# Optimization experiments

Measured on AMD Instinct MI355X. Metric: run time of the kernel, lower is better.

Reference implementation:

```python
import jax, jax.numpy as jnp
import numpy as np

B, N, D = 512, 64, 2
NODE_H, EDGE_H, STEPS, JH = 32, 32, 2, 16
OMEGA = 1.0
ENV_WIDTH = 1.0


def setup_inputs() -> dict:
    key = jax.random.key(0)
    ks = jax.random.split(key, 24)

    def p(k, shape, scale=0.1):
        return jax.random.normal(k, shape, dtype=jnp.float32) * scale

    inp = {}
    inp["x"] = jax.random.normal(ks[0], (B, N, D), dtype=jnp.float32)
    inp["spin"] = jax.random.randint(ks[1], (N,), 0, 2)
    inp["node_W"] = p(ks[2], (NODE_H, D))
    inp["edge_W"] = p(ks[3], (EDGE_H, 1 + 2 * NODE_H))
    inp["rho_ve_W"] = p(ks[4], (STEPS, EDGE_H, NODE_H))
    inp["eu_W1"] = p(ks[5], (STEPS, EDGE_H, 3 * EDGE_H))
    inp["eu_b1"] = p(ks[6], (STEPS, EDGE_H))
    inp["eu_W2"] = p(ks[7], (STEPS, EDGE_H, EDGE_H))
    inp["eu_b2"] = p(ks[8], (STEPS, EDGE_H))
    inp["rho_ev_W"] = p(ks[9], (STEPS, NODE_H, EDGE_H))
    inp["nu_W1"] = p(ks[10], (STEPS, NODE_H, 2 * NODE_H))
    inp["nu_b1"] = p(ks[11], (STEPS, NODE_H))
    inp["nu_W2"] = p(ks[12], (STEPS, NODE_H, NODE_H))
    inp["nu_b2"] = p(ks[13], (STEPS, NODE_H))
    inp["dx_W"] = p(ks[14], (D, NODE_H))
    inp["bf_scale_raw"] = jnp.asarray(np.log(np.exp(1.0) - 1.0), dtype=jnp.float32)
    inp["f_W1"] = p(ks[15], (JH, NODE_H + EDGE_H + 1))
    inp["f_b1"] = p(ks[16], (JH,))
    inp["f_W2"] = p(ks[17], (1, JH))
    inp["f_b2"] = p(ks[18], (1,))
    return inp


def reference(x, spin, node_W, edge_W, rho_ve_W, eu_W1, eu_b1, eu_W2, eu_b2,
              rho_ev_W, nu_W1, nu_b1, nu_W2, nu_b2, dx_W, bf_scale_raw,
              f_W1, f_b1, f_W2, f_b2):
    ii, jj = np.triu_indices(N, k=1)  # upper-triangular pair indices (static)
    x_sc = x * (OMEGA ** 0.5)
    h_v = x_sc @ node_W.T                                   # (B,N,NODE_H)
    r_vec = x_sc[:, None, :, :] - x_sc[:, :, None, :]       # (B,N,N,D)
    r2 = jnp.sum(r_vec * r_vec, axis=-1, keepdims=True)     # (B,N,N,1)
    r1 = jnp.sqrt(r2 + 1e-12)
    h_i = jnp.broadcast_to(h_v[:, :, None, :], (B, N, N, NODE_H))
    h_j = jnp.broadcast_to(h_v[:, None, :, :], (B, N, N, NODE_H))
    h_e = jnp.concatenate([r1, h_i, h_j], axis=-1) @ edge_W.T  # (B,N,N,EDGE_H)

    for s in range(STEPS):
        v = h_v @ rho_ve_W[s].T                              # (B,N,EDGE_H)
        v_i = jnp.broadcast_to(v[:, :, None, :], h_e.shape)
        v_j = jnp.broadcast_to(v[:, None, :, :], h_e.shape)
        ein = jnp.concatenate([h_e, v_i, v_j], axis=-1)      # (B,N,N,3*EDGE_H)
        h_e = jnp.tanh(ein @ eu_W1[s].T + eu_b1[s]) @ eu_W2[s].T + eu_b2[s]
        m_v = jnp.sum(h_e @ rho_ev_W[s].T, axis=2)           # sum aggregation over j
        nin = jnp.concatenate([h_v, m_v], axis=-1)
        h_v = jnp.tanh(nin @ nu_W1[s].T + nu_b1[s]) @ nu_W2[s].T + nu_b2[s]

    scale = jax.nn.softplus(bf_scale_raw)
    dx = scale * jnp.tanh(h_v @ dx_W.T)                      # (B,N,D)

    h_v_mean = h_v.mean(axis=1)                              # (B,NODE_H)
    h_e_mean = h_e[:, ii, jj, :].mean(axis=1)                # (B,EDGE_H)
    rdist = jnp.sqrt(r2[..., 0] + 1e-12)
    mask = 1.0 - jnp.eye(N, dtype=x.dtype)
    r2_mean = jnp.sum(rdist * mask, axis=(1, 2)) / float(N * (N - 1))
    f_in = jnp.concatenate([h_v_mean, h_e_mean, r2_mean[:, None]], axis=-1)
    f_nn = jnp.tanh(f_in @ f_W1.T + f_b1) @ f_W2.T + f_b2    # (B,1)

    ell2 = ENV_WIDTH / max(OMEGA, 1e-12)
    envelope = jnp.exp(-0.5 * jnp.sum(x * x, axis=(1, 2)) / ell2)[:, None]
    diff = x[:, ii, :] - x[:, jj, :]
    r_phys = jnp.sqrt(jnp.sum(diff * diff, axis=-1) + 1e-30)  # (B,P)
    same = (spin[ii] == spin[jj]).astype(x.dtype)
    gamma_para = 1.0 / (D + 1)
    gamma_apara = 1.0 / max(D - 1, 1)
    gamma = same * gamma_para + (1.0 - same) * gamma_apara
    cusp_len = 1.0 / (OMEGA ** 0.5)
    cusp = jnp.sum(gamma * r_phys / (1.0 + r_phys / cusp_len), axis=-1, keepdims=True)
    f = f_nn * envelope + 0.2 * cusp
    return dx, f
```

## Files before the change

kernel.cpp:

```cpp
#include <hip/hip_runtime.h>
#include <math.h>


constexpr float SQRT_OMEGA  = 1.0f;
constexpr float ELL2        = 1.0f;
constexpr float GAMMA_PARA  = 1.0f/3.0f;
constexpr float GAMMA_APARA = 1.0f;
constexpr float C2LOG2E     = 2.8853900817779268f;

typedef float f32x16 __attribute__((ext_vector_type(16)));
typedef short s16x8  __attribute__((ext_vector_type(8)));
typedef unsigned u32x2 __attribute__((ext_vector_type(2)));

__device__ __forceinline__ float ftanh(float x) {
    float e = __expf(2.0f*x);
    return 1.0f - 2.0f/(e + 1.0f);
}

__device__ __forceinline__ float tanhE(float q) {
    float E, r;
    asm("v_exp_f32 %0, %1" : "=v"(E) : "v"(q));
    float d = 1.0f + E;
    asm("v_rcp_f32 %0, %1" : "=v"(r) : "v"(d));
    return fmaf(-2.0f, r, 1.0f);
}

__device__ __forceinline__ unsigned cvtpk(float lo, float hi) {
    unsigned r;
    asm("v_cvt_pk_bf16_f32 %0, %1, %2" : "=v"(r) : "v"(lo), "v"(hi));
    return r;
}

__device__ __forceinline__ s16x8 frag4(unsigned a, unsigned b, unsigned c, unsigned d) {
    union { unsigned u[4]; s16x8 v; } x;
    x.u[0]=a; x.u[1]=b; x.u[2]=c; x.u[3]=d;
    return x.v;
}

#define MFMA(a,b,c) __builtin_amdgcn_mfma_f32_32x32x16_bf16(a,b,c,0,0,0)

__global__ void k_weights(const float* __restrict__ edge_W, const float* __restrict__ rho_ve_W,
                          const float* __restrict__ eu_W1, const float* __restrict__ eu_W2,
                          const float* __restrict__ eu_b2, const float* __restrict__ rho_ev_W,
                          const float* __restrict__ nu_W1, const float* __restrict__ nu_W2,
                          float* __restrict__ MiT0, float* __restrict__ MjT0,
                          float* __restrict__ NiT1, float* __restrict__ NjT1,
                          float* __restrict__ K1T,  float* __restrict__ R0T,
                          float* __restrict__ R1T,  float* __restrict__ rb0,
                          float* __restrict__ rb1,  float* __restrict__ u0c1,
                          float* __restrict__ W1T0, float* __restrict__ W1T1,
                          float* __restrict__ W2T0, float* __restrict__ W2T1)
{
    int t = blockIdx.x*256 + threadIdx.x;
    if (t >= 1024) return;
    int k = t >> 5, eo = t & 31;
    float mi=0.f, mj=0.f, ni=0.f, nj=0.f, k1=0.f;
    for (int a = 0; a < 32; ++a) {
        float w1h = eu_W1[eo*96 + a];
        mi += w1h*edge_W[a*65 + 1 + k];
        mj += w1h*edge_W[a*65 + 33 + k];
        float r0 = rho_ve_W[a*32 + k];
        mi += eu_W1[eo*96 + 32 + a]*r0;
        mj += eu_W1[eo*96 + 64 + a]*r0;
        float r1v = rho_ve_W[1024 + a*32 + k];
        ni += eu_W1[3072 + eo*96 + 32 + a]*r1v;
        nj += eu_W1[3072 + eo*96 + 64 + a]*r1v;
        k1 += eu_W1[3072 + eo*96 + a]*eu_W2[a*32 + k];
    }
    MiT0[t]=mi; MjT0[t]=mj; NiT1[t]=ni; NjT1[t]=nj;
    K1T[t]=k1*C2LOG2E;
    {
        int a = t >> 5, kk = t & 31;
        float r0a=0.f, r1a=0.f;
        for (int e = 0; e < 32; ++e) {
            r0a += rho_ev_W[a*32 + e]*eu_W2[e*32 + kk];
            r1a += rho_ev_W[1024 + a*32 + e]*eu_W2[1024 + e*32 + kk];
        }
        R0T[kk*32 + a] = r0a;
        R1T[kk*32 + a] = r1a;
    }
    {
        int kk = t >> 5, hh = t & 31;
        W1T0[t]        = nu_W1[hh*64 + kk]*C2LOG2E;
        W1T0[1024 + t] = nu_W1[hh*64 + 32 + kk]*C2LOG2E;
        W1T1[t]        = nu_W1[2048 + hh*64 + kk]*C2LOG2E;
        W1T1[1024 + t] = nu_W1[2048 + hh*64 + 32 + kk]*C2LOG2E;
        W2T0[t]        = nu_W2[hh*32 + kk];
        W2T1[t]        = nu_W2[1024 + hh*32 + kk];
    }
    if (t < 32) {
        float u=0.f, c=0.f, b0=0.f, b1v=0.f;
        for (int kk = 0; kk < 32; ++kk) {
            u   += eu_W1[t*96 + kk]*edge_W[kk*65];
            c   += eu_W1[3072 + t*96 + kk]*eu_b2[kk];
            b0  += rho_ev_W[t*32 + kk]*eu_b2[kk];
            b1v += rho_ev_W[1024 + t*32 + kk]*eu_b2[32 + kk];
        }
        u0c1[t] = u*C2LOG2E;
        u0c1[32+t] = c;
        rb0[t] = 64.f*b0; rb1[t] = 64.f*b1v;
    }
}

__launch_bounds__(256)
__global__ void k_fused(const float* __restrict__ x, const int* __restrict__ spin,
                        const float* __restrict__ node_W,
                        const float* __restrict__ eu_b1, const float* __restrict__ eu_W2,
                        const float* __restrict__ eu_b2,
                        const float* __restrict__ MiT0, const float* __restrict__ MjT0,
                        const float* __restrict__ NiT1, const float* __restrict__ NjT1,
                        const float* __restrict__ K1T,  const float* __restrict__ u0c1,
                        const float* __restrict__ R0T,  const float* __restrict__ R1T,
                        const float* __restrict__ rb0,  const float* __restrict__ rb1,
                        const float* __restrict__ W1T0, const float* __restrict__ W1T1,
                        const float* __restrict__ W2T0, const float* __restrict__ W2T1,
                        const float* __restrict__ nu_b1, const float* __restrict__ nu_b2,
                        const float* __restrict__ dx_W, const float* __restrict__ bf_scale,
                        const float* __restrict__ f_W1, const float* __restrict__ f_b1,
                        const float* __restrict__ f_W2, const float* __restrict__ f_b2,
                        float* __restrict__ dx_out, float* __restrict__ f_out)
{
    constexpr int X    = 0;
    constexpr int TI0  = 128;
    constexpr int TJ0  = 2432;
    constexpr int HV   = 4736;
    constexpr int SS   = 6848;
    constexpr int MM   = 8960;
    constexpr int HD   = 11072;
    constexpr int TI1  = MM;
    constexpr int TJ1  = HD;
    constexpr int PART = 128;
    constexpr int RED  = 392;
    constexpr int T1F  = 648;
    constexpr int HVM  = 680;
    constexpr int HEM  = 712;
    __shared__ __align__(16) float sm[13376];
    __shared__ int sp[64];

    const int tid = threadIdx.x;
    const int b   = blockIdx.x;
    const int i   = tid & 63;
    const int c   = tid >> 6;
    const int h   = i >> 5;
    const int n   = i & 31;

    if (tid < 128) sm[X + tid] = x[b*128 + tid]*SQRT_OMEGA;
    if (tid < 64)  sp[tid] = spin[tid];
    __syncthreads();

    for (int out = tid; out < 2048; out += 256) {
        int nn = out >> 5, k = out & 31;
        sm[HV + nn*33 + k] = sm[X + 2*nn]*node_W[k*2] + sm[X + 2*nn + 1]*node_W[k*2+1];
    }
    __syncthreads();

    for (int out = tid; out < 2048; out += 256) {
        int nn = out & 63, e = out >> 6;
        float ai = eu_b1[e], aj = 0.f;
        #pragma unroll
        for (int k = 0; k < 32; ++k) {
            float hvv = sm[HV + nn*33 + k];
            ai += MiT0[k*32 + e]*hvv;
            aj += MjT0[k*32 + e]*hvv;
        }
        sm[TI0 + nn*36 + e] = ai*C2LOG2E;
        sm[TJ0 + nn*36 + e] = aj*C2LOG2E;
    }
    __syncthreads();

    const float xi0 = sm[X + 2*i], xi1 = sm[X + 2*i + 1];

    {
        float ti0v[32];
        #pragma unroll
        for (int q = 0; q < 8; ++q) {
            float4 v = *(const float4*)&sm[TI0 + i*36 + 4*q];
            ti0v[4*q]=v.x; ti0v[4*q+1]=v.y; ti0v[4*q+2]=v.z; ti0v[4*q+3]=v.w;
        }
        float S0[32];
        #pragma unroll
        for (int e = 0; e < 32; ++e) S0[e] = 0.f;
        #pragma unroll 1
        for (int jl = 0; jl < 16; ++jl) {
            const int j = c*16 + jl;
            float d0 = sm[X + 2*j] - xi0;
            float d1 = sm[X + 2*j + 1] - xi1;
            float r1 = sqrtf(d0*d0 + d1*d1 + 1e-12f);
            float tj0v[32];
            #pragma unroll
            for (int q = 0; q < 8; ++q) {
                float4 v = *(const float4*)&sm[TJ0 + j*36 + 4*q];
                tj0v[4*q]=v.x; tj0v[4*q+1]=v.y; tj0v[4*q+2]=v.z; tj0v[4*q+3]=v.w;
            }
            #pragma unroll
            for (int e = 0; e < 32; ++e)
                S0[e] += tanhE(fmaf(r1, u0c1[e], ti0v[e] + tj0v[e]));
        }
        __syncthreads();
        for (int cc = 0; cc < 4; ++cc) {
            if (c == cc) {
                #pragma unroll
                for (int e = 0; e < 32; ++e) {
                    if (cc == 0) sm[SS + i*33 + e]  = S0[e];
                    else         sm[SS + i*33 + e] += S0[e];
                }
            }
            __syncthreads();
        }
    }

    for (int out = tid; out < 2048; out += 256) {
        int nn = out >> 5, a = out & 31;
        float acc = rb0[a];
        #pragma unroll
        for (int k = 0; k < 32; ++k) acc += sm[SS + nn*33 + k]*R0T[k*32 + a];
        sm[MM + nn*33 + a] = acc;
    }
    __syncthreads();
    for (int out = tid; out < 2048; out += 256) {
        int nn = out >> 5, hh = out & 31;
        float acc = nu_b1[hh]*C2LOG2E;
        #pragma unroll
        for (int k = 0; k < 32; ++k) acc += sm[HV + nn*33 + k]*W1T0[k*32 + hh];
        #pragma unroll
        for (int k = 0; k < 32; ++k) acc += sm[MM + nn*33 + k]*W1T0[(32+k)*32 + hh];
        sm[HD + nn*33 + hh] = tanhE(acc);
    }
    __syncthreads();
    for (int out = tid; out < 2048; out += 256) {
        int nn = out >> 5, oo = out & 31;
        float acc = nu_b2[oo];
        #pragma unroll
        for (int k = 0; k < 32; ++k) acc += sm[HD + nn*33 + k]*W2T0[k*32 + oo];
        sm[HV + nn*33 + oo] = acc;
    }
    __syncthreads();

    for (int out = tid; out < 2048; out += 256) {
        int nn = out & 63, e = out >> 6;
        float ai = eu_b1[32 + e] + u0c1[32 + e], aj = 0.f;
        #pragma unroll
        for (int k = 0; k < 32; ++k) {
            float hvv = sm[HV + nn*33 + k];
            ai += NiT1[k*32 + e]*hvv;
            aj += NjT1[k*32 + e]*hvv;
        }
        sm[TI1 + e*65 + nn] = ai*C2LOG2E;
        sm[TJ1 + nn*36 + e] = aj*C2LOG2E;
    }
    __syncthreads();

    {
        s16x8 B1f, B2f;
        {
            unsigned bw[8];
            #pragma unroll
            for (int v = 0; v < 4; ++v) {
                bw[v]   = cvtpk(K1T[(8*h + 2*v)*32 + n],      K1T[(8*h + 2*v + 1)*32 + n]);
                bw[4+v] = cvtpk(K1T[(16 + 8*h + 2*v)*32 + n], K1T[(16 + 8*h + 2*v + 1)*32 + n]);
            }
            B1f = frag4(bw[0],bw[1],bw[2],bw[3]);
            B2f = frag4(bw[4],bw[5],bw[6],bw[7]);
        }
        float ti0v[32];
        #pragma unroll
        for (int q = 0; q < 8; ++q) {
            float4 v = *(const float4*)&sm[TI0 + i*36 + 4*q];
            ti0v[4*q]=v.x; ti0v[4*q+1]=v.y; ti0v[4*q+2]=v.z; ti0v[4*q+3]=v.w;
        }
        float ti1a[16], ti1b[16];
        #pragma unroll
        for (int r = 0; r < 16; ++r) {
            int m = (r&3) + 8*(r>>2) + 4*h;
            ti1a[r] = sm[TI1 + n*65 + m];
            ti1b[r] = sm[TI1 + n*65 + 32 + m];
        }

        float S1a[16], S1b[16];
        #pragma unroll
        for (int r = 0; r < 16; ++r) { S1a[r] = 0.f; S1b[r] = 0.f; }
        float t1acc0 = 0.f, t1acc1 = 0.f;

        #pragma unroll 1
        for (int jl = 0; jl < 16; ++jl) {
            const int j = c*16 + jl;
            float d0 = sm[X + 2*j] - xi0;
            float d1 = sm[X + 2*j + 1] - xi1;
            float r1 = sqrtf(d0*d0 + d1*d1 + 1e-12f);

            float tj0v[32];
            #pragma unroll
            for (int q = 0; q < 8; ++q) {
                float4 v = *(const float4*)&sm[TJ0 + j*36 + 4*q];
                tj0v[4*q]=v.x; tj0v[4*q+1]=v.y; tj0v[4*q+2]=v.z; tj0v[4*q+3]=v.w;
            }
            unsigned w[16];
            #pragma unroll
            for (int q = 0; q < 16; ++q) {
                int e0 = 2*q, e1 = 2*q + 1;
                float ta = tanhE(fmaf(r1, u0c1[e0], ti0v[e0] + tj0v[e0]));
                float tb = tanhE(fmaf(r1, u0c1[e1], ti0v[e1] + tj0v[e1]));
                w[q] = cvtpk(ta, tb);
            }
            unsigned a10[4], a11[4], a20[4], a21[4];
            #pragma unroll
            for (int v = 0; v < 4; ++v) {
                u32x2 ra = __builtin_amdgcn_permlane32_swap(w[v],   w[4+v],  false, false);
                a10[v] = ra[0]; a11[v] = ra[1];
                u32x2 rb = __builtin_amdgcn_permlane32_swap(w[8+v], w[12+v], false, false);
                a20[v] = rb[0]; a21[v] = rb[1];
            }
            float tj1v = sm[TJ1 + j*36 + n];
            f32x16 acc0, acc1;
            #pragma unroll
            for (int r = 0; r < 16; ++r) {
                acc0[r] = ti1a[r] + tj1v;
                acc1[r] = ti1b[r] + tj1v;
            }
            acc0 = MFMA(frag4(a10[0],a10[1],a10[2],a10[3]), B1f, acc0);
            acc0 = MFMA(frag4(a20[0],a20[1],a20[2],a20[3]), B2f, acc0);
            acc1 = MFMA(frag4(a11[0],a11[1],a11[2],a11[3]), B1f, acc1);
            acc1 = MFMA(frag4(a21[0],a21[1],a21[2],a21[3]), B2f, acc1);
            #pragma unroll
            for (int r = 0; r < 16; ++r) {
                int m = (r&3) + 8*(r>>2) + 4*h;
                float t1a = tanhE(acc0[r]);
                float t1b = tanhE(acc1[r]);
                S1a[r] += t1a;
                S1b[r] += t1b;
                if (j > m)      t1acc0 += t1a;
                if (j > 32 + m) t1acc1 += t1b;
            }
        }
        __syncthreads();

        {
            float tf = t1acc0 + t1acc1;
            tf += __shfl_xor(tf, 32, 64);
            if (i < 32) sm[PART + c*33 + i] = tf;
        }
        for (int cc = 0; cc < 4; ++cc) {
            if (c == cc) {
                #pragma unroll
                for (int r = 0; r < 16; ++r) {
                    int m = (r&3) + 8*(r>>2) + 4*h;
                    if (cc == 0) {
                        sm[SS + m*33 + n]        = S1a[r];
                        sm[SS + (32+m)*33 + n]   = S1b[r];
                    } else {
                        sm[SS + m*33 + n]       += S1a[r];
                        sm[SS + (32+m)*33 + n]  += S1b[r];
                    }
                }
            }
            __syncthreads();
        }
        if (tid < 32) {
            sm[T1F + tid] = sm[PART + tid] + sm[PART + 33 + tid]
                          + sm[PART + 66 + tid] + sm[PART + 99 + tid];
        }
        __syncthreads();
    }

    for (int out = tid; out < 2048; out += 256) {
        int nn = out >> 5, a = out & 31;
        float acc = rb1[a];
        #pragma unroll
        for (int k = 0; k < 32; ++k) acc += sm[SS + nn*33 + k]*R1T[k*32 + a];
        sm[MM + nn*33 + a] = acc;
    }
    __syncthreads();
    for (int out = tid; out < 2048; out += 256) {
        int nn = out >> 5, hh = out & 31;
        float acc = nu_b1[32 + hh]*C2LOG2E;
        #pragma unroll
        for (int k = 0; k < 32; ++k) acc += sm[HV + nn*33 + k]*W1T1[k*32 + hh];
        #pragma unroll
        for (int k = 0; k < 32; ++k) acc += sm[MM + nn*33 + k]*W1T1[(32+k)*32 + hh];
        sm[HD + nn*33 + hh] = tanhE(acc);
    }
    __syncthreads();
    for (int out = tid; out < 2048; out += 256) {
        int nn = out >> 5, oo = out & 31;
        float acc = nu_b2[32 + oo];
        #pragma unroll
        for (int k = 0; k < 32; ++k) acc += sm[HD + nn*33 + k]*W2T1[k*32 + oo];
        sm[MM + nn*33 + oo] = acc;
    }
    __syncthreads();

    if (tid < 128) {
        int nn = tid >> 1, d = tid & 1;
        float scale = log1pf(__expf(bf_scale[0]));
        float a = 0.f;
        #pragma unroll
        for (int k = 0; k < 32; ++k) a += sm[MM + nn*33 + k]*dx_W[d*32 + k];
        dx_out[(b*64 + nn)*2 + d] = scale*ftanh(a);
    }
    {
        int e = tid & 31, g = tid >> 5;
        float p = 0.f;
        #pragma unroll
        for (int r = 0; r < 8; ++r) p += sm[MM + (g*8 + r)*33 + e];
        sm[PART + g*33 + e] = p;
    }
    __syncthreads();
    if (tid < 32) {
        float s = 0.f;
        #pragma unroll
        for (int g = 0; g < 8; ++g) s += sm[PART + g*33 + tid];
        sm[HVM + tid] = s*(1.0f/64.0f);
        float he = 0.f;
        #pragma unroll
        for (int k = 0; k < 32; ++k) he += eu_W2[1024 + tid*32 + k]*sm[T1F + k];
        sm[HEM + tid] = he*(1.0f/2016.0f) + eu_b2[32 + tid];
    }

    float rsum = 0.f, cusp = 0.f, env = 0.f;
    for (int idx = tid; idx < 4096; idx += 256) {
        int ii = idx >> 6, jj = idx & 63;
        if (ii < jj) {
            float d0 = sm[X + ii*2] - sm[X + jj*2];
            float d1 = sm[X + ii*2 + 1] - sm[X + jj*2 + 1];
            float r2 = d0*d0 + d1*d1;
            rsum += sqrtf(r2 + 1e-12f);
            float rp = sqrtf(r2 + 1e-30f);
            float gamma = (sp[ii] == sp[jj]) ? GAMMA_PARA : GAMMA_APARA;
            cusp += gamma*rp/(1.0f + rp*SQRT_OMEGA);
        }
    }
    if (tid < 128) { float v = sm[X + tid]; env = v*v; }

    auto blockReduce = [&](float v) -> float {
        sm[RED + tid] = v; __syncthreads();
        for (int s = 128; s > 0; s >>= 1) {
            if (tid < s) sm[RED + tid] += sm[RED + tid + s];
            __syncthreads();
        }
        float r = sm[RED]; __syncthreads(); return r;
    };
    float rtot = blockReduce(rsum);
    float ctot = blockReduce(cusp);
    float etot = blockReduce(env);

    if (tid < 16) {
        float r2m = rtot*(1.0f/2016.0f);
        float envelope = __expf(-0.5f*etot/ELL2);
        float acc = f_b1[tid];
        #pragma unroll
        for (int m2 = 0; m2 < 32; ++m2) acc += sm[HVM + m2]*f_W1[tid*65 + m2];
        #pragma unroll
        for (int m2 = 0; m2 < 32; ++m2) acc += sm[HEM + m2]*f_W1[tid*65 + 32 + m2];
        acc += r2m*f_W1[tid*65 + 64];
        float v = ftanh(acc)*f_W2[tid];
        v += __shfl_xor(v, 8, 64);
        v += __shfl_xor(v, 4, 64);
        v += __shfl_xor(v, 2, 64);
        v += __shfl_xor(v, 1, 64);
        if (tid == 0) f_out[b] = (v + f_b2[0])*envelope + 0.2f*ctot;
    }
}

extern "C" void kernel_launch(void* const* d_in, const int* in_sizes, int n_in,
                              void* d_out, int out_size, void* d_ws, size_t ws_size,
                              hipStream_t stream)
{
    (void)in_sizes; (void)n_in; (void)out_size; (void)ws_size;
    const float* x         = (const float*)d_in[0];
    const int*   spin      = (const int*)d_in[1];
    const float* node_W    = (const float*)d_in[2];
    const float* edge_W    = (const float*)d_in[3];
    const float* rho_ve_W  = (const float*)d_in[4];
    const float* eu_W1     = (const float*)d_in[5];
    const float* eu_b1     = (const float*)d_in[6];
    const float* eu_W2     = (const float*)d_in[7];
    const float* eu_b2     = (const float*)d_in[8];
    const float* rho_ev_W  = (const float*)d_in[9];
    const float* nu_W1     = (const float*)d_in[10];
    const float* nu_b1     = (const float*)d_in[11];
    const float* nu_W2     = (const float*)d_in[12];
    const float* nu_b2     = (const float*)d_in[13];
    const float* dx_W      = (const float*)d_in[14];
    const float* bf_scale  = (const float*)d_in[15];
    const float* f_W1      = (const float*)d_in[16];
    const float* f_b1      = (const float*)d_in[17];
    const float* f_W2      = (const float*)d_in[18];
    const float* f_b2      = (const float*)d_in[19];

    float* ws    = (float*)d_ws;
    float* MiT0  = ws;
    float* MjT0  = MiT0 + 1024;
    float* NiT1  = MjT0 + 1024;
    float* NjT1  = NiT1 + 1024;
    float* K1T   = NjT1 + 1024;
    float* R0T   = K1T  + 1024;
    float* R1T   = R0T  + 1024;
    float* W1T0  = R1T  + 1024;
    float* W1T1  = W1T0 + 2048;
    float* W2T0  = W1T1 + 2048;
    float* W2T1  = W2T0 + 1024;
    float* rb0   = W2T1 + 1024;
    float* rb1   = rb0  + 32;
    float* u0c1  = rb1  + 32;

    float* dxout = (float*)d_out;
    float* fout  = dxout + 512*64*2;

    k_weights<<<4, 256, 0, stream>>>(edge_W, rho_ve_W, eu_W1, eu_W2, eu_b2, rho_ev_W,
                                     nu_W1, nu_W2,
                                     MiT0, MjT0, NiT1, NjT1, K1T, R0T, R1T,
                                     rb0, rb1, u0c1, W1T0, W1T1, W2T0, W2T1);
    k_fused<<<512, 256, 0, stream>>>(x, spin, node_W, eu_b1, eu_W2, eu_b2,
                                     MiT0, MjT0, NiT1, NjT1, K1T, u0c1,
                                     R0T, R1T, rb0, rb1, W1T0, W1T1, W2T0, W2T1,
                                     nu_b1, nu_b2, dx_W, bf_scale,
                                     f_W1, f_b1, f_W2, f_b2, dxout, fout);
}
```

Before: 208.8 us.

## Fold weight-precompute kernel into fused kernel, computing combined weights per block in LDS

Removes the separate k_weights launch and its workspace. Each of the 512 blocks now recomputes the combined edge-update weight matrices (Mi/Mj, Ni/Nj, K1, u0/c1) into shared memory and applies rho_ev, eu_W2 and nu weights directly instead of using pre-fused products. This drops one kernel launch and the dependency between the two kernels, but every block now does redundant weight matmuls that read global memory, and it adds extra matmul passes and barriers.

```diff
diff --git a/kernel.cpp b/kernel.cpp
--- a/kernel.cpp
+++ b/kernel.cpp
@@ -39,83 +39,22 @@
 
 #define MFMA(a,b,c) __builtin_amdgcn_mfma_f32_32x32x16_bf16(a,b,c,0,0,0)
 
-__global__ void k_weights(const float* __restrict__ edge_W, const float* __restrict__ rho_ve_W,
-                          const float* __restrict__ eu_W1, const float* __restrict__ eu_W2,
-                          const float* __restrict__ eu_b2, const float* __restrict__ rho_ev_W,
-                          const float* __restrict__ nu_W1, const float* __restrict__ nu_W2,
-                          float* __restrict__ MiT0, float* __restrict__ MjT0,
-                          float* __restrict__ NiT1, float* __restrict__ NjT1,
-                          float* __restrict__ K1T,  float* __restrict__ R0T,
-                          float* __restrict__ R1T,  float* __restrict__ rb0,
-                          float* __restrict__ rb1,  float* __restrict__ u0c1,
-                          float* __restrict__ W1T0, float* __restrict__ W1T1,
-                          float* __restrict__ W2T0, float* __restrict__ W2T1)
-{
-    int t = blockIdx.x*256 + threadIdx.x;
-    if (t >= 1024) return;
-    int k = t >> 5, eo = t & 31;
-    float mi=0.f, mj=0.f, ni=0.f, nj=0.f, k1=0.f;
-    for (int a = 0; a < 32; ++a) {
-        float w1h = eu_W1[eo*96 + a];
-        mi += w1h*edge_W[a*65 + 1 + k];
-        mj += w1h*edge_W[a*65 + 33 + k];
-        float r0 = rho_ve_W[a*32 + k];
-        mi += eu_W1[eo*96 + 32 + a]*r0;
-        mj += eu_W1[eo*96 + 64 + a]*r0;
-        float r1v = rho_ve_W[1024 + a*32 + k];
-        ni += eu_W1[3072 + eo*96 + 32 + a]*r1v;
-        nj += eu_W1[3072 + eo*96 + 64 + a]*r1v;
-        k1 += eu_W1[3072 + eo*96 + a]*eu_W2[a*32 + k];
-    }
-    MiT0[t]=mi; MjT0[t]=mj; NiT1[t]=ni; NjT1[t]=nj;
-    K1T[t]=k1*C2LOG2E;
-    {
-        int a = t >> 5, kk = t & 31;
-        float r0a=0.f, r1a=0.f;
-        for (int e = 0; e < 32; ++e) {
-            r0a += rho_ev_W[a*32 + e]*eu_W2[e*32 + kk];
-            r1a += rho_ev_W[1024 + a*32 + e]*eu_W2[1024 + e*32 + kk];
-        }
-        R0T[kk*32 + a] = r0a;
-        R1T[kk*32 + a] = r1a;
-    }
-    {
-        int kk = t >> 5, hh = t & 31;
-        W1T0[t]        = nu_W1[hh*64 + kk]*C2LOG2E;
-        W1T0[1024 + t] = nu_W1[hh*64 + 32 + kk]*C2LOG2E;
-        W1T1[t]        = nu_W1[2048 + hh*64 + kk]*C2LOG2E;
-        W1T1[1024 + t] = nu_W1[2048 + hh*64 + 32 + kk]*C2LOG2E;
-        W2T0[t]        = nu_W2[hh*32 + kk];
-        W2T1[t]        = nu_W2[1024 + hh*32 + kk];
-    }
-    if (t < 32) {
-        float u=0.f, c=0.f, b0=0.f, b1v=0.f;
-        for (int kk = 0; kk < 32; ++kk) {
-            u   += eu_W1[t*96 + kk]*edge_W[kk*65];
-            c   += eu_W1[3072 + t*96 + kk]*eu_b2[kk];
-            b0  += rho_ev_W[t*32 + kk]*eu_b2[kk];
-            b1v += rho_ev_W[1024 + t*32 + kk]*eu_b2[32 + kk];
-        }
-        u0c1[t] = u*C2LOG2E;
-        u0c1[32+t] = c;
-        rb0[t] = 64.f*b0; rb1[t] = 64.f*b1v;
-    }
-}
-
 __launch_bounds__(256)
 __global__ void k_fused(const float* __restrict__ x, const int* __restrict__ spin,
                         const float* __restrict__ node_W,
-                        const float* __restrict__ eu_b1, const float* __restrict__ eu_W2,
+                        const float* __restrict__ edge_W,
+                        const float* __restrict__ rho_ve_W,
+                        const float* __restrict__ eu_W1,
+                        const float* __restrict__ eu_b1,
+                        const float* __restrict__ eu_W2,
                         const float* __restrict__ eu_b2,
-                        const float* __restrict__ MiT0, const float* __restrict__ MjT0,
-                        const float* __restrict__ NiT1, const float* __restrict__ NjT1,
-                        const float* __restrict__ K1T,  const float* __restrict__ u0c1,
-                        const float* __restrict__ R0T,  const float* __restrict__ R1T,
-                        const float* __restrict__ rb0,  const float* __restrict__ rb1,
-                        const float* __restrict__ W1T0, const float* __restrict__ W1T1,
-                        const float* __restrict__ W2T0, const float* __restrict__ W2T1,
-                        const float* __restrict__ nu_b1, const float* __restrict__ nu_b2,
-                        const float* __restrict__ dx_W, const float* __restrict__ bf_scale,
+                        const float* __restrict__ rho_ev_W,
+                        const float* __restrict__ nu_W1,
+                        const float* __restrict__ nu_b1,
+                        const float* __restrict__ nu_W2,
+                        const float* __restrict__ nu_b2,
+                        const float* __restrict__ dx_W,
+                        const float* __restrict__ bf_scale,
                         const float* __restrict__ f_W1, const float* __restrict__ f_b1,
                         const float* __restrict__ f_W2, const float* __restrict__ f_b2,
                         float* __restrict__ dx_out, float* __restrict__ f_out)
@@ -129,12 +68,13 @@
     constexpr int HD   = 11072;
     constexpr int TI1  = MM;
     constexpr int TJ1  = HD;
+    constexpr int U0C1 = 13376;
     constexpr int PART = 128;
     constexpr int RED  = 392;
     constexpr int T1F  = 648;
     constexpr int HVM  = 680;
     constexpr int HEM  = 712;
-    __shared__ __align__(16) float sm[13376];
+    __shared__ __align__(16) float sm[13440];
     __shared__ int sp[64];
 
     const int tid = threadIdx.x;
@@ -152,6 +92,31 @@
         int nn = out >> 5, k = out & 31;
         sm[HV + nn*33 + k] = sm[X + 2*nn]*node_W[k*2] + sm[X + 2*nn + 1]*node_W[k*2+1];
     }
+
+    for (int out = tid; out < 2048; out += 256) {
+        int tb = out >> 10, idx = out & 1023;
+        int eo = idx >> 5, k = idx & 31;
+        float acc = 0.f;
+        if (tb == 0) {
+            for (int a = 0; a < 32; ++a)
+                acc += eu_W1[eo*96 + a]*edge_W[a*65 + 1 + k]
+                     + eu_W1[eo*96 + 32 + a]*rho_ve_W[a*32 + k];
+        } else {
+            for (int a = 0; a < 32; ++a)
+                acc += eu_W1[eo*96 + a]*edge_W[a*65 + 33 + k]
+                     + eu_W1[eo*96 + 64 + a]*rho_ve_W[a*32 + k];
+        }
+        sm[MM + tb*1024 + eo*32 + k] = acc;
+    }
+    if (tid < 32) {
+        float u = 0.f, cc1 = 0.f;
+        for (int kk = 0; kk < 32; ++kk) {
+            u   += eu_W1[tid*96 + kk]*edge_W[kk*65];
+            cc1 += eu_W1[3072 + tid*96 + kk]*eu_b2[kk];
+        }
+        sm[U0C1 + tid]      = u*C2LOG2E;
+        sm[U0C1 + 32 + tid] = cc1;
+    }
     __syncthreads();
 
     for (int out = tid; out < 2048; out += 256) {
@@ -160,8 +125,8 @@
         #pragma unroll
         for (int k = 0; k < 32; ++k) {
             float hvv = sm[HV + nn*33 + k];
-            ai += MiT0[k*32 + e]*hvv;
-            aj += MjT0[k*32 + e]*hvv;
+            ai += sm[MM + e*32 + k]*hvv;
+            aj += sm[MM + 1024 + e*32 + k]*hvv;
         }
         sm[TI0 + nn*36 + e] = ai*C2LOG2E;
         sm[TJ0 + nn*36 + e] = aj*C2LOG2E;
@@ -194,7 +159,7 @@
             }
             #pragma unroll
             for (int e = 0; e < 32; ++e)
-                S0[e] += tanhE(fmaf(r1, u0c1[e], ti0v[e] + tj0v[e]));
+                S0[e] += tanhE(fmaf(r1, sm[U0C1 + e], ti0v[e] + tj0v[e]));
         }
         __syncthreads();
         for (int cc = 0; cc < 4; ++cc) {
@@ -210,43 +175,75 @@
     }
 
     for (int out = tid; out < 2048; out += 256) {
+        int nn = out >> 5, e = out & 31;
+        float acc = 64.f*eu_b2[e];
+        #pragma unroll
+        for (int k = 0; k < 32; ++k) acc += sm[SS + nn*33 + k]*eu_W2[e*32 + k];
+        sm[MM + nn*33 + e] = acc;
+    }
+    __syncthreads();
+    for (int out = tid; out < 2048; out += 256) {
         int nn = out >> 5, a = out & 31;
-        float acc = rb0[a];
-        #pragma unroll
-        for (int k = 0; k < 32; ++k) acc += sm[SS + nn*33 + k]*R0T[k*32 + a];
-        sm[MM + nn*33 + a] = acc;
+        float acc = 0.f;
+        #pragma unroll
+        for (int e = 0; e < 32; ++e) acc += rho_ev_W[a*32 + e]*sm[MM + nn*33 + e];
+        sm[HD + nn*33 + a] = acc;
     }
     __syncthreads();
     for (int out = tid; out < 2048; out += 256) {
         int nn = out >> 5, hh = out & 31;
-        float acc = nu_b1[hh]*C2LOG2E;
-        #pragma unroll
-        for (int k = 0; k < 32; ++k) acc += sm[HV + nn*33 + k]*W1T0[k*32 + hh];
-        #pragma unroll
-        for (int k = 0; k < 32; ++k) acc += sm[MM + nn*33 + k]*W1T0[(32+k)*32 + hh];
-        sm[HD + nn*33 + hh] = tanhE(acc);
+        float acc = nu_b1[hh];
+        #pragma unroll
+        for (int k = 0; k < 32; ++k) acc += sm[HV + nn*33 + k]*nu_W1[hh*64 + k];
+        #pragma unroll
+        for (int k = 0; k < 32; ++k) acc += sm[HD + nn*33 + k]*nu_W1[hh*64 + 32 + k];
+        sm[SS + nn*33 + hh] = tanhE(acc*C2LOG2E);
     }
     __syncthreads();
     for (int out = tid; out < 2048; out += 256) {
         int nn = out >> 5, oo = out & 31;
         float acc = nu_b2[oo];
         #pragma unroll
-        for (int k = 0; k < 32; ++k) acc += sm[HD + nn*33 + k]*W2T0[k*32 + oo];
+        for (int k = 0; k < 32; ++k) acc += sm[SS + nn*33 + k]*nu_W2[oo*32 + k];
         sm[HV + nn*33 + oo] = acc;
     }
     __syncthreads();
 
     for (int out = tid; out < 2048; out += 256) {
+        int tb = out >> 10, idx = out & 1023;
+        int eo = idx >> 5, k = idx & 31;
+        float acc = 0.f;
+        if (tb == 0) {
+            for (int a = 0; a < 32; ++a)
+                acc += eu_W1[3072 + eo*96 + 32 + a]*rho_ve_W[1024 + a*32 + k];
+        } else {
+            for (int a = 0; a < 32; ++a)
+                acc += eu_W1[3072 + eo*96 + 64 + a]*rho_ve_W[1024 + a*32 + k];
+        }
+        sm[SS + tb*1024 + eo*32 + k] = acc;
+    }
+    __syncthreads();
+
+    for (int out = tid; out < 2048; out += 256) {
         int nn = out & 63, e = out >> 6;
-        float ai = eu_b1[32 + e] + u0c1[32 + e], aj = 0.f;
+        float ai = eu_b1[32 + e] + sm[U0C1 + 32 + e], aj = 0.f;
         #pragma unroll
         for (int k = 0; k < 32; ++k) {
             float hvv = sm[HV + nn*33 + k];
-            ai += NiT1[k*32 + e]*hvv;
-            aj += NjT1[k*32 + e]*hvv;
+            ai += sm[SS + e*32 + k]*hvv;
+            aj += sm[SS + 1024 + e*32 + k]*hvv;
         }
         sm[TI1 + e*65 + nn] = ai*C2LOG2E;
         sm[TJ1 + nn*36 + e] = aj*C2LOG2E;
+    }
+    __syncthreads();
+
+    for (int out = tid; out < 1024; out += 256) {
+        int eo = out & 31, k = out >> 5;
+        float acc = 0.f;
+        for (int a = 0; a < 32; ++a)
+            acc += eu_W1[3072 + eo*96 + a]*eu_W2[a*32 + k];
+        sm[SS + k*32 + eo] = acc*C2LOG2E;
     }
     __syncthreads();
 
@@ -256,8 +253,8 @@
             unsigned bw[8];
             #pragma unroll
             for (int v = 0; v < 4; ++v) {
-                bw[v]   = cvtpk(K1T[(8*h + 2*v)*32 + n],      K1T[(8*h + 2*v + 1)*32 + n]);
-                bw[4+v] = cvtpk(K1T[(16 + 8*h + 2*v)*32 + n], K1T[(16 + 8*h + 2*v + 1)*32 + n]);
+                bw[v]   = cvtpk(sm[SS + (8*h + 2*v)*32 + n],      sm[SS + (8*h + 2*v + 1)*32 + n]);
+                bw[4+v] = cvtpk(sm[SS + (16 + 8*h + 2*v)*32 + n], sm[SS + (16 + 8*h + 2*v + 1)*32 + n]);
             }
             B1f = frag4(bw[0],bw[1],bw[2],bw[3]);
             B2f = frag4(bw[4],bw[5],bw[6],bw[7]);
@@ -298,8 +295,8 @@
             #pragma unroll
             for (int q = 0; q < 16; ++q) {
                 int e0 = 2*q, e1 = 2*q + 1;
-                float ta = tanhE(fmaf(r1, u0c1[e0], ti0v[e0] + tj0v[e0]));
-                float tb = tanhE(fmaf(r1, u0c1[e1], ti0v[e1] + tj0v[e1]));
+                float ta = tanhE(fmaf(r1, sm[U0C1 + e0], ti0v[e0] + tj0v[e0]));
+                float tb = tanhE(fmaf(r1, sm[U0C1 + e1], ti0v[e1] + tj0v[e1]));
                 w[q] = cvtpk(ta, tb);
             }
             unsigned a10[4], a11[4], a20[4], a21[4];
@@ -363,28 +360,36 @@
     }
 
     for (int out = tid; out < 2048; out += 256) {
+        int nn = out >> 5, e = out & 31;
+        float acc = 64.f*eu_b2[32 + e];
+        #pragma unroll
+        for (int k = 0; k < 32; ++k) acc += sm[SS + nn*33 + k]*eu_W2[1024 + e*32 + k];
+        sm[MM + nn*33 + e] = acc;
+    }
+    __syncthreads();
+    for (int out = tid; out < 2048; out += 256) {
         int nn = out >> 5, a = out & 31;
-        float acc = rb1[a];
-        #pragma unroll
-        for (int k = 0; k < 32; ++k) acc += sm[SS + nn*33 + k]*R1T[k*32 + a];
-        sm[MM + nn*33 + a] = acc;
+        float acc = 0.f;
+        #pragma unroll
+        for (int e = 0; e < 32; ++e) acc += rho_ev_W[1024 + a*32 + e]*sm[MM + nn*33 + e];
+        sm[HD + nn*33 + a] = acc;
     }
     __syncthreads();
     for (int out = tid; out < 2048; out += 256) {
         int nn = out >> 5, hh = out & 31;
-        float acc = nu_b1[32 + hh]*C2LOG2E;
-        #pragma unroll
-        for (int k = 0; k < 32; ++k) acc += sm[HV + nn*33 + k]*W1T1[k*32 + hh];
-        #pragma unroll
-        for (int k = 0; k < 32; ++k) acc += sm[MM + nn*33 + k]*W1T1[(32+k)*32 + hh];
-        sm[HD + nn*33 + hh] = tanhE(acc);
+        float acc = nu_b1[32 + hh];
+        #pragma unroll
+        for (int k = 0; k < 32; ++k) acc += sm[HV + nn*33 + k]*nu_W1[2048 + hh*64 + k];
+        #pragma unroll
+        for (int k = 0; k < 32; ++k) acc += sm[HD + nn*33 + k]*nu_W1[2048 + hh*64 + 32 + k];
+        sm[SS + nn*33 + hh] = tanhE(acc*C2LOG2E);
     }
     __syncthreads();
     for (int out = tid; out < 2048; out += 256) {
         int nn = out >> 5, oo = out & 31;
         float acc = nu_b2[32 + oo];
         #pragma unroll
-        for (int k = 0; k < 32; ++k) acc += sm[HD + nn*33 + k]*W2T1[k*32 + oo];
+        for (int k = 0; k < 32; ++k) acc += sm[SS + nn*33 + k]*nu_W2[1024 + oo*32 + k];
         sm[MM + nn*33 + oo] = acc;
     }
     __syncthreads();
@@ -465,7 +470,7 @@
                               void* d_out, int out_size, void* d_ws, size_t ws_size,
                               hipStream_t stream)
 {
-    (void)in_sizes; (void)n_in; (void)out_size; (void)ws_size;
+    (void)in_sizes; (void)n_in; (void)out_size; (void)d_ws; (void)ws_size;
     const float* x         = (const float*)d_in[0];
     const int*   spin      = (const int*)d_in[1];
     const float* node_W    = (const float*)d_in[2];
@@ -487,32 +492,12 @@
     const float* f_W2      = (const float*)d_in[18];
     const float* f_b2      = (const float*)d_in[19];
 
-    float* ws    = (float*)d_ws;
-    float* MiT0  = ws;
-    float* MjT0  = MiT0 + 1024;
-    float* NiT1  = MjT0 + 1024;
-    float* NjT1  = NiT1 + 1024;
-    float* K1T   = NjT1 + 1024;
-    float* R0T   = K1T  + 1024;
-    float* R1T   = R0T  + 1024;
-    float* W1T0  = R1T  + 1024;
-    float* W1T1  = W1T0 + 2048;
-    float* W2T0  = W1T1 + 2048;
-    float* W2T1  = W2T0 + 1024;
-    float* rb0   = W2T1 + 1024;
-    float* rb1   = rb0  + 32;
-    float* u0c1  = rb1  + 32;
-
     float* dxout = (float*)d_out;
     float* fout  = dxout + 512*64*2;
 
-    k_weights<<<4, 256, 0, stream>>>(edge_W, rho_ve_W, eu_W1, eu_W2, eu_b2, rho_ev_W,
-                                     nu_W1, nu_W2,
-                                     MiT0, MjT0, NiT1, NjT1, K1T, R0T, R1T,
-                                     rb0, rb1, u0c1, W1T0, W1T1, W2T0, W2T1);
-    k_fused<<<512, 256, 0, stream>>>(x, spin, node_W, eu_b1, eu_W2, eu_b2,
-                                     MiT0, MjT0, NiT1, NjT1, K1T, u0c1,
-                                     R0T, R1T, rb0, rb1, W1T0, W1T1, W2T0, W2T1,
-                                     nu_b1, nu_b2, dx_W, bf_scale,
-                                     f_W1, f_b1, f_W2, f_b2, dxout, fout);
+    k_fused<<<512, 256, 0, stream>>>(x, spin, node_W, edge_W, rho_ve_W,
+                                     eu_W1, eu_b1, eu_W2, eu_b2, rho_ev_W,
+                                     nu_W1, nu_b1, nu_W2, nu_b2,
+                                     dx_W, bf_scale, f_W1, f_b1, f_W2, f_b2,
+                                     dxout, fout);
 }
```

New measurement: 315.1 us. 1.51x slower.
